# Performance work log

Hardware: AMD Instinct MI355X
Metric: run time of the kernel (lower is better)

Reference implementation:

```python
import jax, jax.numpy as jnp
import numpy as np

B, L, H, HEADS, BLOCKS, TSPAN = 8, 256, 256, 4, 2, 512
D = H // HEADS
BIG_NEG = jnp.float32(-2.0**32 + 1)


def _layernorm(x, g, b, eps=1e-8):
    m = x.mean(-1, keepdims=True)
    v = ((x - m) ** 2).mean(-1, keepdims=True)
    return (x - m) / jnp.sqrt(v + eps) * g + b


def _forward(seq_emb, Wq, bq, Wk, bk, Wv, bv, ln1_g, ln1_b, ln2_g, ln2_b,
             W1, b1, W2, b2, pos_K, pos_V, tK_emb, tV_emb, lnf_g, lnf_b,
             mask, time_matrices):
    # relative time-interval embeddings: [B,L,L,H] -> per-head [B,L,L,heads,D]
    tmKh = tK_emb[time_matrices].reshape(B, L, L, HEADS, D)
    tmVh = tV_emb[time_matrices].reshape(B, L, L, HEADS, D)
    posKh = pos_K.reshape(L, HEADS, D)  # abs position embs (positions = arange(L))
    posVh = pos_V.reshape(L, HEADS, D)
    keep = (~mask)[..., None].astype(seq_emb.dtype)  # [B,L,1], True mask = pad
    causal = ~jnp.tril(jnp.ones((L, L), dtype=bool))  # True above diagonal
    x = seq_emb * keep
    scale = jnp.sqrt(jnp.float32(D))
    for i in range(BLOCKS):
        q = _layernorm(x, ln1_g[i], ln1_b[i])  # queries normalized, keys/values raw
        Qh = (q @ Wq[i].T + bq[i]).reshape(B, L, HEADS, D)
        Kh = (x @ Wk[i].T + bk[i]).reshape(B, L, HEADS, D)
        Vh = (x @ Wv[i].T + bv[i]).reshape(B, L, HEADS, D)
        aw = (jnp.einsum('bqhd,bkhd->bhqk', Qh, Kh)
              + jnp.einsum('bqhd,khd->bhqk', Qh, posKh)
              + jnp.einsum('bqhd,bqkhd->bhqk', Qh, tmKh)) / scale
        aw = jnp.where(mask[:, None, :, None] | causal[None, None], BIG_NEG, aw)
        p = jax.nn.softmax(aw, axis=-1)
        out = (jnp.einsum('bhqk,bkhd->bqhd', p, Vh)
               + jnp.einsum('bhqk,khd->bqhd', p, posVh)
               + jnp.einsum('bhqk,bqkhd->bqhd', p, tmVh)).reshape(B, L, H)
        x = q + out
        x = _layernorm(x, ln2_g[i], ln2_b[i])
        h = jax.nn.relu(jnp.einsum('bld,od->blo', x, W1[i]) + b1[i])  # Conv1d k=1 == Linear
        x = jnp.einsum('bld,od->blo', h, W2[i]) + b2[i] + x
        x = x * keep
    return _layernorm(x, lnf_g, lnf_b)


def setup_inputs():
    key = jax.random.key(0)
    ks = jax.random.split(key, 24)
    s = 0.02
    nrm = lambda k, shape: jax.random.normal(k, shape, dtype=jnp.float32) * s
    inp = {}
    inp['mask'] = jax.random.uniform(ks[0], (B, L)) < 0.1
    inp['seq_emb'] = jax.random.normal(ks[1], (B, L, H), dtype=jnp.float32)
    inp['log_seqs'] = jax.random.randint(ks[2], (B, L), 0, 1000)
    inp['time_matrices'] = jax.random.randint(ks[3], (B, L, L), 0, TSPAN + 1).astype(jnp.int32)
    inp['time_attn'] = 0
    inp['Wq'] = nrm(ks[4], (BLOCKS, H, H)); inp['bq'] = jnp.zeros((BLOCKS, H), jnp.float32)
    inp['Wk'] = nrm(ks[5], (BLOCKS, H, H)); inp['bk'] = jnp.zeros((BLOCKS, H), jnp.float32)
    inp['Wv'] = nrm(ks[6], (BLOCKS, H, H)); inp['bv'] = jnp.zeros((BLOCKS, H), jnp.float32)
    inp['ln1_g'] = jnp.ones((BLOCKS, H), jnp.float32); inp['ln1_b'] = jnp.zeros((BLOCKS, H), jnp.float32)
    inp['ln2_g'] = jnp.ones((BLOCKS, H), jnp.float32); inp['ln2_b'] = jnp.zeros((BLOCKS, H), jnp.float32)
    inp['W1'] = nrm(ks[7], (BLOCKS, H, H)); inp['b1'] = jnp.zeros((BLOCKS, H), jnp.float32)
    inp['W2'] = nrm(ks[8], (BLOCKS, H, H)); inp['b2'] = jnp.zeros((BLOCKS, H), jnp.float32)
    inp['pos_K'] = nrm(ks[9], (L, H)); inp['pos_V'] = nrm(ks[10], (L, H))
    inp['tK_emb'] = nrm(ks[11], (TSPAN + 1, H)); inp['tV_emb'] = nrm(ks[12], (TSPAN + 1, H))
    inp['lnf_g'] = jnp.ones((H,), jnp.float32); inp['lnf_b'] = jnp.zeros((H,), jnp.float32)
    return inp


def reference(mask, seq_emb, log_seqs, time_matrices, time_attn,
              Wq, bq, Wk, bk, Wv, bv, ln1_g, ln1_b, ln2_g, ln2_b,
              W1, b1, W2, b2, pos_K, pos_V, tK_emb, tV_emb, lnf_g, lnf_b):
    return _forward(seq_emb, Wq, bq, Wk, bk, Wv, bv, ln1_g, ln1_b, ln2_g, ln2_b,
                    W1, b1, W2, b2, pos_K, pos_V, tK_emb, tV_emb, lnf_g, lnf_b,
                    mask, time_matrices)
```

## Files before the change

### kernel.cpp

```cpp
#include <hip/hip_runtime.h>

#define BIG_NEG_F (-4294967296.0f)

typedef __attribute__((ext_vector_type(8))) short bf16x8;
typedef __attribute__((ext_vector_type(4))) float f32x4;

__device__ __forceinline__ float wave_sum(float v) {
#pragma unroll
    for (int m = 32; m; m >>= 1) v += __shfl_xor(v, m, 64);
    return v;
}
__device__ __forceinline__ float wave_max(float v) {
#pragma unroll
    for (int m = 32; m; m >>= 1) v = fmaxf(v, __shfl_xor(v, m, 64));
    return v;
}

__device__ __forceinline__ unsigned int pack2(float a, float b) {
    return (__float_as_uint(b) & 0xffff0000u) | (__float_as_uint(a) >> 16);
}
__device__ __forceinline__ float hipart(float x) {
    return __uint_as_float(__float_as_uint(x) & 0xffff0000u);
}
__device__ __forceinline__ void store_pair(unsigned short* hp, unsigned short* lp,
                                           float4 a, float4 b) {
    uint4 h;
    h.x = pack2(a.x, a.y); h.y = pack2(a.z, a.w);
    h.z = pack2(b.x, b.y); h.w = pack2(b.z, b.w);
    float lax = a.x - hipart(a.x), lay = a.y - hipart(a.y);
    float laz = a.z - hipart(a.z), law = a.w - hipart(a.w);
    float lbx = b.x - hipart(b.x), lby = b.y - hipart(b.y);
    float lbz = b.z - hipart(b.z), lbw = b.w - hipart(b.w);
    uint4 l;
    l.x = pack2(lax, lay); l.y = pack2(laz, law);
    l.z = pack2(lbx, lby); l.w = pack2(lbz, lbw);
    *(uint4*)hp = h;
    *(uint4*)lp = l;
}

__global__ __launch_bounds__(256) void prep_ln_kernel(const float* __restrict__ seq,
                                                      const unsigned char* __restrict__ mraw,
                                                      unsigned char* __restrict__ mout,
                                                      float* __restrict__ X, float* __restrict__ Q,
                                                      const float* __restrict__ g,
                                                      const float* __restrict__ be) {
    __shared__ int flags[2];
    __shared__ float ws[8];
    int row = blockIdx.x, tid = threadIdx.x;
    if (tid == 0) { flags[0] = 0; flags[1] = 0; }
    __syncthreads();
    for (int i = tid; i < 2048; i += 256) {
        if (mraw[i]) {
            if (i & 3) atomicOr(&flags[0], 1);
            else if (i & 4) atomicOr(&flags[1], 1);
        }
    }
    __syncthreads();
    int mode = flags[0] ? 0 : (flags[1] ? 1 : 2);
    unsigned char mrow = (mode == 0) ? mraw[row] : (mode == 1) ? mraw[row * 4] : mraw[row * 8];
    if (tid == 0) mout[row] = mrow ? 1 : 0;
    int idx = row * 256 + tid;
    int w = tid >> 6, lane = tid & 63;
    float v = mrow ? 0.f : seq[idx];
    X[idx] = v;
    float s = wave_sum(v);
    if (lane == 0) ws[w] = s;
    __syncthreads();
    float mean = (ws[0] + ws[1] + ws[2] + ws[3]) * (1.f / 256.f);
    float d = v - mean;
    float s2 = wave_sum(d * d);
    if (lane == 0) ws[4 + w] = s2;
    __syncthreads();
    float var = (ws[4] + ws[5] + ws[6] + ws[7]) * (1.f / 256.f);
    Q[idx] = d / sqrtf(var + 1e-8f) * g[tid] + be[tid];
}

__global__ __launch_bounds__(256) void ln_kernel(const float* __restrict__ X, float* __restrict__ Y,
                                                 const float* __restrict__ g,
                                                 const float* __restrict__ be) {
    __shared__ float ws[8];
    int row = blockIdx.x, tid = threadIdx.x;
    int idx = row * 256 + tid;
    int w = tid >> 6, lane = tid & 63;
    float v = X[idx];
    float s = wave_sum(v);
    if (lane == 0) ws[w] = s;
    __syncthreads();
    float mean = (ws[0] + ws[1] + ws[2] + ws[3]) * (1.f / 256.f);
    float d = v - mean;
    float s2 = wave_sum(d * d);
    if (lane == 0) ws[4 + w] = s2;
    __syncthreads();
    float var = (ws[4] + ws[5] + ws[6] + ws[7]) * (1.f / 256.f);
    Y[idx] = d / sqrtf(var + 1e-8f) * g[tid] + be[tid];
}

struct GemmJob {
    const float* A;
    const float* W;
    const float* bias;
    const float* pos;
    const float* res;
    const unsigned char* maskm;
    float* C;
    int relu;
};

__global__ __launch_bounds__(256) void gemm_mfma_kernel(GemmJob j0, GemmJob j1, GemmJob j2) {
    GemmJob J = (blockIdx.z == 0) ? j0 : (blockIdx.z == 1 ? j1 : j2);
    __shared__ unsigned short Ah[32][72], Al[32][72], Wh[64][72], Wl[64][72];
    int tid = threadIdx.x;
    int n0 = blockIdx.x * 64, m0 = blockIdx.y * 32;
    int w = tid >> 6, lane = tid & 63;
    int wm = w >> 1, wn = w & 1;
    int rowA = tid >> 3, kA = (tid & 7) * 8;
    int rowW = tid >> 2, kW = (tid & 3) * 16;
    const float* Asrc = J.A + (m0 + rowA) * 256 + kA;
    const float* Wsrc = J.W + (n0 + rowW) * 256 + kW;
    float4 ar0 = *(const float4*)(Asrc), ar1 = *(const float4*)(Asrc + 4);
    float4 wr0 = *(const float4*)(Wsrc),      wr1 = *(const float4*)(Wsrc + 4),
           wr2 = *(const float4*)(Wsrc + 8),  wr3 = *(const float4*)(Wsrc + 12);
    f32x4 acc[2] = {};
    int r15 = lane & 15, hgrp = (lane >> 4) << 3;
    for (int kt = 0; kt < 4; ++kt) {
        if (kt) __syncthreads();
        store_pair(&Ah[rowA][kA],     &Al[rowA][kA],     ar0, ar1);
        store_pair(&Wh[rowW][kW],     &Wl[rowW][kW],     wr0, wr1);
        store_pair(&Wh[rowW][kW + 8], &Wl[rowW][kW + 8], wr2, wr3);
        __syncthreads();
        if (kt < 3) {
            int ko = (kt + 1) * 64;
            ar0 = *(const float4*)(Asrc + ko);      ar1 = *(const float4*)(Asrc + ko + 4);
            wr0 = *(const float4*)(Wsrc + ko);      wr1 = *(const float4*)(Wsrc + ko + 4);
            wr2 = *(const float4*)(Wsrc + ko + 8);  wr3 = *(const float4*)(Wsrc + ko + 12);
        }
#pragma unroll
        for (int s = 0; s < 2; ++s) {
            int ko = s * 32 + hgrp;
            bf16x8 ah = *(const bf16x8*)&Ah[wm * 16 + r15][ko];
            bf16x8 al = *(const bf16x8*)&Al[wm * 16 + r15][ko];
            bf16x8 bh0 = *(const bf16x8*)&Wh[wn * 32 + r15][ko];
            bf16x8 bh1 = *(const bf16x8*)&Wh[wn * 32 + 16 + r15][ko];
            bf16x8 bl0 = *(const bf16x8*)&Wl[wn * 32 + r15][ko];
            bf16x8 bl1 = *(const bf16x8*)&Wl[wn * 32 + 16 + r15][ko];
            acc[0] = __builtin_amdgcn_mfma_f32_16x16x32_bf16(ah, bh0, acc[0], 0, 0, 0);
            acc[0] = __builtin_amdgcn_mfma_f32_16x16x32_bf16(ah, bl0, acc[0], 0, 0, 0);
            acc[0] = __builtin_amdgcn_mfma_f32_16x16x32_bf16(al, bh0, acc[0], 0, 0, 0);
            acc[1] = __builtin_amdgcn_mfma_f32_16x16x32_bf16(ah, bh1, acc[1], 0, 0, 0);
            acc[1] = __builtin_amdgcn_mfma_f32_16x16x32_bf16(ah, bl1, acc[1], 0, 0, 0);
            acc[1] = __builtin_amdgcn_mfma_f32_16x16x32_bf16(al, bh1, acc[1], 0, 0, 0);
        }
    }
#pragma unroll
    for (int nf = 0; nf < 2; ++nf) {
        int col = n0 + wn * 32 + nf * 16 + r15;
        int rowb = m0 + wm * 16 + ((lane >> 4) << 2);
        float bcol = J.bias[col];
        f32x4 a = acc[nf];
#pragma unroll
        for (int rr = 0; rr < 4; ++rr) {
            int m = rowb + rr;
            float v = a[rr] + bcol;
            if (J.pos) v += J.pos[(m & 255) * 256 + col];
            if (J.relu) v = fmaxf(v, 0.f);
            if (J.res) v += J.res[m * 256 + col];
            if (J.maskm && J.maskm[m]) v = 0.f;
            J.C[m * 256 + col] = v;
        }
    }
}

__global__ __launch_bounds__(256, 4) void attn_kernel(
    const float* __restrict__ Q, const float* __restrict__ Kp, const float* __restrict__ Vp,
    const float* __restrict__ qres, const int* __restrict__ tm,
    const float* __restrict__ tK, const float* __restrict__ tV,
    const float* __restrict__ g2, const float* __restrict__ b2,
    float* __restrict__ X2) {
    int bid = (int)blockIdx.x;
    int b = bid & 7;
    int i6 = bid >> 3;
    int j = i6 & 31, a = i6 >> 5;
    int base = 2 * j + (a >> 1);
    int P = (a & 1) ? base : 127 - base;
    int qA = 2 * P, qB = 2 * P + 1;
    int tid = threadIdx.x, w = tid >> 6, lane = tid & 63;
    __shared__ float qrow[2][256];
    __shared__ int   stm[2][256];
    __shared__ float p[2][4][264];
    __shared__ float opart[2][4][256];
    __shared__ float denom[2][4];
    __shared__ float lnws[2][8];

    int rowbaseA = (b * 256 + qA) * 256;
    int rowbaseB = (b * 256 + qB) * 256;
    qrow[0][tid] = Q[rowbaseA + tid];
    qrow[1][tid] = Q[rowbaseB + tid];
    {
        int tA = tm[rowbaseA + tid];
        int tB = tm[rowbaseB + tid];
        stm[0][tid] = tA < 0 ? 0 : (tA > 512 ? 512 : tA);
        stm[1][tid] = tB < 0 ? 0 : (tB > 512 ? 512 : tB);
    }
    __syncthreads();

    {
        int h = lane >> 4;
        const float* qrA = &qrow[0][lane * 4];
        const float* qrB = &qrow[1][lane * 4];
        float qA0 = qrA[0], qA1 = qrA[1], qA2 = qrA[2], qA3 = qrA[3];
        float qB0 = qrB[0], qB1 = qrB[1], qB2 = qrB[2], qB3 = qrB[3];
        const float* Kb  = Kp + (size_t)(b << 8) * 256 + lane * 4;
        const float* tKb = tK + lane * 4;
        int nact = (qB >= w) ? ((qB - w) >> 2) + 1 : 0;
        int i = 0;
        for (; i + 2 <= nact; i += 2) {
            int k0 = w + 4 * i, k1 = k0 + 4;
            float4 kv0 = *(const float4*)(Kb + k0 * 256);
            float4 kv1 = *(const float4*)(Kb + k1 * 256);
            float4 tA0 = *(const float4*)(tKb + stm[0][k0] * 256);
            float4 tA1 = *(const float4*)(tKb + stm[0][k1] * 256);
            float4 tB0 = *(const float4*)(tKb + stm[1][k0] * 256);
            float4 tB1 = *(const float4*)(tKb + stm[1][k1] * 256);
            float sA0 = qA0 * (kv0.x + tA0.x) + qA1 * (kv0.y + tA0.y) + qA2 * (kv0.z + tA0.z) + qA3 * (kv0.w + tA0.w);
            float sA1 = qA0 * (kv1.x + tA1.x) + qA1 * (kv1.y + tA1.y) + qA2 * (kv1.z + tA1.z) + qA3 * (kv1.w + tA1.w);
            float sB0 = qB0 * (kv0.x + tB0.x) + qB1 * (kv0.y + tB0.y) + qB2 * (kv0.z + tB0.z) + qB3 * (kv0.w + tB0.w);
            float sB1 = qB0 * (kv1.x + tB1.x) + qB1 * (kv1.y + tB1.y) + qB2 * (kv1.z + tB1.z) + qB3 * (kv1.w + tB1.w);
            sA0 += __shfl_xor(sA0, 1, 64); sA1 += __shfl_xor(sA1, 1, 64);
            sB0 += __shfl_xor(sB0, 1, 64); sB1 += __shfl_xor(sB1, 1, 64);
            sA0 += __shfl_xor(sA0, 2, 64); sA1 += __shfl_xor(sA1, 2, 64);
            sB0 += __shfl_xor(sB0, 2, 64); sB1 += __shfl_xor(sB1, 2, 64);
            sA0 += __shfl_xor(sA0, 4, 64); sA1 += __shfl_xor(sA1, 4, 64);
            sB0 += __shfl_xor(sB0, 4, 64); sB1 += __shfl_xor(sB1, 4, 64);
            sA0 += __shfl_xor(sA0, 8, 64); sA1 += __shfl_xor(sA1, 8, 64);
            sB0 += __shfl_xor(sB0, 8, 64); sB1 += __shfl_xor(sB1, 8, 64);
            if ((lane & 15) == 0) {
                p[0][h][k0] = sA0 * 0.125f;
                p[0][h][k1] = sA1 * 0.125f;
                p[1][h][k0] = sB0 * 0.125f;
                p[1][h][k1] = sB1 * 0.125f;
            }
        }
        if (i < nact) {
            int k = w + 4 * i;
            float4 kv = *(const float4*)(Kb + k * 256);
            float4 tA4 = *(const float4*)(tKb + stm[0][k] * 256);
            float4 tB4 = *(const float4*)(tKb + stm[1][k] * 256);
            float sA = qA0 * (kv.x + tA4.x) + qA1 * (kv.y + tA4.y) + qA2 * (kv.z + tA4.z) + qA3 * (kv.w + tA4.w);
            float sB = qB0 * (kv.x + tB4.x) + qB1 * (kv.y + tB4.y) + qB2 * (kv.z + tB4.z) + qB3 * (kv.w + tB4.w);
            sA += __shfl_xor(sA, 1, 64); sB += __shfl_xor(sB, 1, 64);
            sA += __shfl_xor(sA, 2, 64); sB += __shfl_xor(sB, 2, 64);
            sA += __shfl_xor(sA, 4, 64); sB += __shfl_xor(sB, 4, 64);
            sA += __shfl_xor(sA, 8, 64); sB += __shfl_xor(sB, 8, 64);
            if ((lane & 15) == 0) {
                p[0][h][k] = sA * 0.125f;
                p[1][h][k] = sB * 0.125f;
            }
        }
    }
    __syncthreads();

    {
        float* phA = &p[0][w][0];
        float* phB = &p[1][w][0];
        float a0 = (lane       <= qA) ? phA[lane      ] : BIG_NEG_F;
        float a1 = (lane + 64  <= qA) ? phA[lane + 64 ] : BIG_NEG_F;
        float a2 = (lane + 128 <= qA) ? phA[lane + 128] : BIG_NEG_F;
        float a3 = (lane + 192 <= qA) ? phA[lane + 192] : BIG_NEG_F;
        float b0 = (lane       <= qB) ? phB[lane      ] : BIG_NEG_F;
        float b1 = (lane + 64  <= qB) ? phB[lane + 64 ] : BIG_NEG_F;
        float b2v = (lane + 128 <= qB) ? phB[lane + 128] : BIG_NEG_F;
        float b3 = (lane + 192 <= qB) ? phB[lane + 192] : BIG_NEG_F;
        float mxA = wave_max(fmaxf(fmaxf(a0, a1), fmaxf(a2, a3)));
        float mxB = wave_max(fmaxf(fmaxf(b0, b1), fmaxf(b2v, b3)));
        float eA0 = (lane       <= qA) ? __expf(a0 - mxA) : 0.f;
        float eA1 = (lane + 64  <= qA) ? __expf(a1 - mxA) : 0.f;
        float eA2 = (lane + 128 <= qA) ? __expf(a2 - mxA) : 0.f;
        float eA3 = (lane + 192 <= qA) ? __expf(a3 - mxA) : 0.f;
        float eB0 = (lane       <= qB) ? __expf(b0 - mxB) : 0.f;
        float eB1 = (lane + 64  <= qB) ? __expf(b1 - mxB) : 0.f;
        float eB2 = (lane + 128 <= qB) ? __expf(b2v - mxB) : 0.f;
        float eB3 = (lane + 192 <= qB) ? __expf(b3 - mxB) : 0.f;
        phA[lane] = eA0; phA[lane + 64] = eA1; phA[lane + 128] = eA2; phA[lane + 192] = eA3;
        phB[lane] = eB0; phB[lane + 64] = eB1; phB[lane + 128] = eB2; phB[lane + 192] = eB3;
        float sumA = wave_sum(eA0 + eA1 + eA2 + eA3);
        float sumB = wave_sum(eB0 + eB1 + eB2 + eB3);
        if (lane == 0) { denom[0][w] = sumA; denom[1][w] = sumB; }
    }
    __syncthreads();

    {
        int hh = lane >> 4;
        const float* Vb  = Vp + (size_t)(b << 8) * 256 + lane * 4;
        const float* tVb = tV + lane * 4;
        const float* prA = &p[0][hh][0];
        const float* prB = &p[1][hh][0];
        float4 aA0 = {0.f, 0.f, 0.f, 0.f}, aA1 = aA0, aB0 = aA0, aB1 = aA0;
        int cnt = (qB >= w) ? ((qB - w) >> 2) + 1 : 0;
        int i = 0;
        for (; i + 2 <= cnt; i += 2) {
            int k0 = w + 4 * i, k1 = k0 + 4;
            float pA0 = prA[k0], pA1 = prA[k1], pB0 = prB[k0], pB1 = prB[k1];
            float4 v0 = *(const float4*)(Vb + k0 * 256);
            float4 v1 = *(const float4*)(Vb + k1 * 256);
            float4 uA0 = *(const float4*)(tVb + stm[0][k0] * 256);
            float4 uA1 = *(const float4*)(tVb + stm[0][k1] * 256);
            float4 uB0 = *(const float4*)(tVb + stm[1][k0] * 256);
            float4 uB1 = *(const float4*)(tVb + stm[1][k1] * 256);
            aA0.x += pA0 * (v0.x + uA0.x); aA0.y += pA0 * (v0.y + uA0.y); aA0.z += pA0 * (v0.z + uA0.z); aA0.w += pA0 * (v0.w + uA0.w);
            aA1.x += pA1 * (v1.x + uA1.x); aA1.y += pA1 * (v1.y + uA1.y); aA1.z += pA1 * (v1.z + uA1.z); aA1.w += pA1 * (v1.w + uA1.w);
            aB0.x += pB0 * (v0.x + uB0.x); aB0.y += pB0 * (v0.y + uB0.y); aB0.z += pB0 * (v0.z + uB0.z); aB0.w += pB0 * (v0.w + uB0.w);
            aB1.x += pB1 * (v1.x + uB1.x); aB1.y += pB1 * (v1.y + uB1.y); aB1.z += pB1 * (v1.z + uB1.z); aB1.w += pB1 * (v1.w + uB1.w);
        }
        if (i < cnt) {
            int k2 = w + 4 * i;
            float pA = prA[k2], pB = prB[k2];
            float4 v = *(const float4*)(Vb + k2 * 256);
            float4 uA = *(const float4*)(tVb + stm[0][k2] * 256);
            float4 uB = *(const float4*)(tVb + stm[1][k2] * 256);
            aA0.x += pA * (v.x + uA.x); aA0.y += pA * (v.y + uA.y);
            aA0.z += pA * (v.z + uA.z); aA0.w += pA * (v.w + uA.w);
            aB0.x += pB * (v.x + uB.x); aB0.y += pB * (v.y + uB.y);
            aB0.z += pB * (v.z + uB.z); aB0.w += pB * (v.w + uB.w);
        }
        float4 oA, oB;
        oA.x = aA0.x + aA1.x; oA.y = aA0.y + aA1.y; oA.z = aA0.z + aA1.z; oA.w = aA0.w + aA1.w;
        oB.x = aB0.x + aB1.x; oB.y = aB0.y + aB1.y; oB.z = aB0.z + aB1.z; oB.w = aB0.w + aB1.w;
        *(float4*)&opart[0][w][lane * 4] = oA;
        *(float4*)&opart[1][w][lane * 4] = oB;
    }
    __syncthreads();

    {
        int d = tid, h = tid >> 6;
        float totA = opart[0][0][d] + opart[0][1][d] + opart[0][2][d] + opart[0][3][d];
        float totB = opart[1][0][d] + opart[1][1][d] + opart[1][2][d] + opart[1][3][d];
        float xvA = qres[rowbaseA + d] + totA / denom[0][h];
        float xvB = qres[rowbaseB + d] + totB / denom[1][h];
        float sA = wave_sum(xvA);
        float sB = wave_sum(xvB);
        if (lane == 0) { lnws[0][w] = sA; lnws[1][w] = sB; }
        __syncthreads();
        float meanA = (lnws[0][0] + lnws[0][1] + lnws[0][2] + lnws[0][3]) * (1.f / 256.f);
        float meanB = (lnws[1][0] + lnws[1][1] + lnws[1][2] + lnws[1][3]) * (1.f / 256.f);
        float ddA = xvA - meanA, ddB = xvB - meanB;
        float s2A = wave_sum(ddA * ddA);
        float s2B = wave_sum(ddB * ddB);
        if (lane == 0) { lnws[0][4 + w] = s2A; lnws[1][4 + w] = s2B; }
        __syncthreads();
        float varA = (lnws[0][4] + lnws[0][5] + lnws[0][6] + lnws[0][7]) * (1.f / 256.f);
        float varB = (lnws[1][4] + lnws[1][5] + lnws[1][6] + lnws[1][7]) * (1.f / 256.f);
        float gg = g2[d], bb = b2[d];
        X2[rowbaseA + d] = ddA / sqrtf(varA + 1e-8f) * gg + bb;
        X2[rowbaseB + d] = ddB / sqrtf(varB + 1e-8f) * gg + bb;
    }
}

extern "C" void kernel_launch(void* const* d_in, const int* in_sizes, int n_in,
                              void* d_out, int out_size, void* d_ws, size_t ws_size,
                              hipStream_t stream) {
    const unsigned char* mask_raw = (const unsigned char*)d_in[0];
    const float* seq  = (const float*)d_in[1];
    const int*   tm   = (const int*)d_in[3];
    const float* Wq   = (const float*)d_in[5];
    const float* bq   = (const float*)d_in[6];
    const float* Wk   = (const float*)d_in[7];
    const float* bk   = (const float*)d_in[8];
    const float* Wv   = (const float*)d_in[9];
    const float* bv   = (const float*)d_in[10];
    const float* ln1g = (const float*)d_in[11];
    const float* ln1b = (const float*)d_in[12];
    const float* ln2g = (const float*)d_in[13];
    const float* ln2b = (const float*)d_in[14];
    const float* W1   = (const float*)d_in[15];
    const float* b1   = (const float*)d_in[16];
    const float* W2   = (const float*)d_in[17];
    const float* b2   = (const float*)d_in[18];
    const float* posK = (const float*)d_in[19];
    const float* posV = (const float*)d_in[20];
    const float* tK   = (const float*)d_in[21];
    const float* tV   = (const float*)d_in[22];
    const float* lnfg = (const float*)d_in[23];
    const float* lnfb = (const float*)d_in[24];

    const int NEL = 8 * 256 * 256;
    float* x   = (float*)d_ws;
    float* q   = x   + NEL;
    float* Qb  = q   + NEL;
    float* KpB = Qb  + NEL;
    float* VpB = KpB + NEL;
    float* x2  = VpB + NEL;
    float* hb  = x2  + NEL;
    unsigned char* mask = (unsigned char*)(hb + NEL);

    dim3 gQKV(4, 64, 3);
    dim3 gFFN(4, 64, 1);

    prep_ln_kernel<<<2048, 256, 0, stream>>>(seq, mask_raw, mask, x, q, ln1g, ln1b);
    for (int blk = 0; blk < 2; ++blk) {
        int o1 = blk * 256, oW = blk * 256 * 256;
        GemmJob jq = {q, Wq + oW, bq + o1, nullptr, nullptr, nullptr, Qb, 0};
        GemmJob jk = {x, Wk + oW, bk + o1, posK,    nullptr, nullptr, KpB, 0};
        GemmJob jv = {x, Wv + oW, bv + o1, posV,    nullptr, nullptr, VpB, 0};
        gemm_mfma_kernel<<<gQKV, 256, 0, stream>>>(jq, jk, jv);
        attn_kernel<<<1024, 256, 0, stream>>>(Qb, KpB, VpB, q, tm, tK, tV,
                                              ln2g + o1, ln2b + o1, x2);
        GemmJob f1 = {x2, W1 + oW, b1 + o1, nullptr, nullptr, nullptr, hb, 1};
        gemm_mfma_kernel<<<gFFN, 256, 0, stream>>>(f1, f1, f1);
        GemmJob f2 = {hb, W2 + oW, b2 + o1, nullptr, x2, mask, x, 0};
        gemm_mfma_kernel<<<gFFN, 256, 0, stream>>>(f2, f2, f2);
        if (blk == 0) ln_kernel<<<2048, 256, 0, stream>>>(x, q, ln1g + 256, ln1b + 256);
    }
    ln_kernel<<<2048, 256, 0, stream>>>(x, (float*)d_out, lnfg, lnfb);
}
```

Baseline: 236.8 us.

## Precompute query-by-time-embedding scores with MFMA and gather them in attention

Adds a kernel that multiplies every query head vector by all 513 time-interval key embeddings using split-bf16 MFMA, writing a per-query, per-head score table. The attention kernel then gathers one scalar per key from this table instead of loading a 4-float tK row per lane and folding it into the dot product. This removes the redundant gathered tK traffic, since only 513 distinct embeddings exist. The cost is an extra launch and a table of 2048x4x516 floats written and read through global memory, plus slight precision loss from the three-term bf16 split.

```diff
diff --git a/kernel.cpp b/kernel.cpp
--- a/kernel.cpp
+++ b/kernel.cpp
@@ -1,6 +1,7 @@
 #include <hip/hip_runtime.h>
 
 #define BIG_NEG_F (-4294967296.0f)
+#define TSTRIDE 516
 
 typedef __attribute__((ext_vector_type(8))) short bf16x8;
 typedef __attribute__((ext_vector_type(4))) float f32x4;
@@ -36,6 +37,17 @@
     l.z = pack2(lbx, lby); l.w = pack2(lbz, lbw);
     *(uint4*)hp = h;
     *(uint4*)lp = l;
+}
+__device__ __forceinline__ void mk_frag(float4 a, float4 b, bf16x8* hi, bf16x8* lo) {
+    uint4 h, l;
+    h.x = pack2(a.x, a.y); h.y = pack2(a.z, a.w);
+    h.z = pack2(b.x, b.y); h.w = pack2(b.z, b.w);
+    l.x = pack2(a.x - hipart(a.x), a.y - hipart(a.y));
+    l.y = pack2(a.z - hipart(a.z), a.w - hipart(a.w));
+    l.z = pack2(b.x - hipart(b.x), b.y - hipart(b.y));
+    l.w = pack2(b.z - hipart(b.z), b.w - hipart(b.w));
+    *hi = *(bf16x8*)&h;
+    *lo = *(bf16x8*)&l;
 }
 
 __global__ __launch_bounds__(256) void prep_ln_kernel(const float* __restrict__ seq,
@@ -170,10 +182,48 @@
     }
 }
 
+__global__ __launch_bounds__(256) void tscore_kernel(const float* __restrict__ Qp,
+                                                     const float* __restrict__ tK,
+                                                     float* __restrict__ T) {
+    int tid = threadIdx.x, w = tid >> 6, lane = tid & 63;
+    int t0 = blockIdx.x * 64 + w * 16;
+    int q0 = blockIdx.y * 16;
+    int h  = blockIdx.z;
+    int r15 = lane & 15, kq = (lane >> 4) << 3;
+    const float* Ap = Qp + (q0 + r15) * 256 + h * 64 + kq;
+    int trow = t0 + r15;
+    const float* Bp = tK + trow * 256 + h * 64 + kq;
+    bool tvalid = trow < 513;
+    f32x4 acc = {0.f, 0.f, 0.f, 0.f};
+#pragma unroll
+    for (int s = 0; s < 2; ++s) {
+        float4 a0 = *(const float4*)(Ap + s * 32);
+        float4 a1 = *(const float4*)(Ap + s * 32 + 4);
+        float4 b0 = {0.f, 0.f, 0.f, 0.f}, b1 = b0;
+        if (tvalid) {
+            b0 = *(const float4*)(Bp + s * 32);
+            b1 = *(const float4*)(Bp + s * 32 + 4);
+        }
+        bf16x8 ah, al, bh, bl;
+        mk_frag(a0, a1, &ah, &al);
+        mk_frag(b0, b1, &bh, &bl);
+        acc = __builtin_amdgcn_mfma_f32_16x16x32_bf16(ah, bh, acc, 0, 0, 0);
+        acc = __builtin_amdgcn_mfma_f32_16x16x32_bf16(ah, bl, acc, 0, 0, 0);
+        acc = __builtin_amdgcn_mfma_f32_16x16x32_bf16(al, bh, acc, 0, 0, 0);
+    }
+    int tcol = t0 + r15;
+    if (tcol < 513) {
+        int qrow = q0 + ((lane >> 4) << 2);
+#pragma unroll
+        for (int rr = 0; rr < 4; ++rr)
+            T[((qrow + rr) * 4 + h) * TSTRIDE + tcol] = acc[rr];
+    }
+}
+
 __global__ __launch_bounds__(256, 4) void attn_kernel(
     const float* __restrict__ Q, const float* __restrict__ Kp, const float* __restrict__ Vp,
     const float* __restrict__ qres, const int* __restrict__ tm,
-    const float* __restrict__ tK, const float* __restrict__ tV,
+    const float* __restrict__ T, const float* __restrict__ tV,
     const float* __restrict__ g2, const float* __restrict__ b2,
     float* __restrict__ X2) {
     int bid = (int)blockIdx.x;
@@ -193,6 +243,7 @@
 
     int rowbaseA = (b * 256 + qA) * 256;
     int rowbaseB = (b * 256 + qB) * 256;
+    int qgA = b * 256 + qA, qgB = b * 256 + qB;
     qrow[0][tid] = Q[rowbaseA + tid];
     qrow[1][tid] = Q[rowbaseB + tid];
     {
@@ -209,22 +260,21 @@
         const float* qrB = &qrow[1][lane * 4];
         float qA0 = qrA[0], qA1 = qrA[1], qA2 = qrA[2], qA3 = qrA[3];
         float qB0 = qrB[0], qB1 = qrB[1], qB2 = qrB[2], qB3 = qrB[3];
-        const float* Kb  = Kp + (size_t)(b << 8) * 256 + lane * 4;
-        const float* tKb = tK + lane * 4;
+        const float* Kb = Kp + (size_t)(b << 8) * 256 + lane * 4;
+        const float* TA = T + (qgA * 4 + h) * TSTRIDE;
+        const float* TB = T + (qgB * 4 + h) * TSTRIDE;
         int nact = (qB >= w) ? ((qB - w) >> 2) + 1 : 0;
         int i = 0;
         for (; i + 2 <= nact; i += 2) {
             int k0 = w + 4 * i, k1 = k0 + 4;
             float4 kv0 = *(const float4*)(Kb + k0 * 256);
             float4 kv1 = *(const float4*)(Kb + k1 * 256);
-            float4 tA0 = *(const float4*)(tKb + stm[0][k0] * 256);
-            float4 tA1 = *(const float4*)(tKb + stm[0][k1] * 256);
-            float4 tB0 = *(const float4*)(tKb + stm[1][k0] * 256);
-            float4 tB1 = *(const float4*)(tKb + stm[1][k1] * 256);
-            float sA0 = qA0 * (kv0.x + tA0.x) + qA1 * (kv0.y + tA0.y) + qA2 * (kv0.z + tA0.z) + qA3 * (kv0.w + tA0.w);
-            float sA1 = qA0 * (kv1.x + tA1.x) + qA1 * (kv1.y + tA1.y) + qA2 * (kv1.z + tA1.z) + qA3 * (kv1.w + tA1.w);
-            float sB0 = qB0 * (kv0.x + tB0.x) + qB1 * (kv0.y + tB0.y) + qB2 * (kv0.z + tB0.z) + qB3 * (kv0.w + tB0.w);
-            float sB1 = qB0 * (kv1.x + tB1.x) + qB1 * (kv1.y + tB1.y) + qB2 * (kv1.z + tB1.z) + qB3 * (kv1.w + tB1.w);
+            float tA0 = TA[stm[0][k0]], tA1 = TA[stm[0][k1]];
+            float tB0 = TB[stm[1][k0]], tB1 = TB[stm[1][k1]];
+            float sA0 = qA0 * kv0.x + qA1 * kv0.y + qA2 * kv0.z + qA3 * kv0.w;
+            float sA1 = qA0 * kv1.x + qA1 * kv1.y + qA2 * kv1.z + qA3 * kv1.w;
+            float sB0 = qB0 * kv0.x + qB1 * kv0.y + qB2 * kv0.z + qB3 * kv0.w;
+            float sB1 = qB0 * kv1.x + qB1 * kv1.y + qB2 * kv1.z + qB3 * kv1.w;
             sA0 += __shfl_xor(sA0, 1, 64); sA1 += __shfl_xor(sA1, 1, 64);
             sB0 += __shfl_xor(sB0, 1, 64); sB1 += __shfl_xor(sB1, 1, 64);
             sA0 += __shfl_xor(sA0, 2, 64); sA1 += __shfl_xor(sA1, 2, 64);
@@ -234,26 +284,25 @@
             sA0 += __shfl_xor(sA0, 8, 64); sA1 += __shfl_xor(sA1, 8, 64);
             sB0 += __shfl_xor(sB0, 8, 64); sB1 += __shfl_xor(sB1, 8, 64);
             if ((lane & 15) == 0) {
-                p[0][h][k0] = sA0 * 0.125f;
-                p[0][h][k1] = sA1 * 0.125f;
-                p[1][h][k0] = sB0 * 0.125f;
-                p[1][h][k1] = sB1 * 0.125f;
+                p[0][h][k0] = (sA0 + tA0) * 0.125f;
+                p[0][h][k1] = (sA1 + tA1) * 0.125f;
+                p[1][h][k0] = (sB0 + tB0) * 0.125f;
+                p[1][h][k1] = (sB1 + tB1) * 0.125f;
             }
         }
         if (i < nact) {
             int k = w + 4 * i;
             float4 kv = *(const float4*)(Kb + k * 256);
-            float4 tA4 = *(const float4*)(tKb + stm[0][k] * 256);
-            float4 tB4 = *(const float4*)(tKb + stm[1][k] * 256);
-            float sA = qA0 * (kv.x + tA4.x) + qA1 * (kv.y + tA4.y) + qA2 * (kv.z + tA4.z) + qA3 * (kv.w + tA4.w);
-            float sB = qB0 * (kv.x + tB4.x) + qB1 * (kv.y + tB4.y) + qB2 * (kv.z + tB4.z) + qB3 * (kv.w + tB4.w);
+            float tA4 = TA[stm[0][k]], tB4 = TB[stm[1][k]];
+            float sA = qA0 * kv.x + qA1 * kv.y + qA2 * kv.z + qA3 * kv.w;
+            float sB = qB0 * kv.x + qB1 * kv.y + qB2 * kv.z + qB3 * kv.w;
             sA += __shfl_xor(sA, 1, 64); sB += __shfl_xor(sB, 1, 64);
             sA += __shfl_xor(sA, 2, 64); sB += __shfl_xor(sB, 2, 64);
             sA += __shfl_xor(sA, 4, 64); sB += __shfl_xor(sB, 4, 64);
             sA += __shfl_xor(sA, 8, 64); sB += __shfl_xor(sB, 8, 64);
             if ((lane & 15) == 0) {
-                p[0][h][k] = sA * 0.125f;
-                p[1][h][k] = sB * 0.125f;
+                p[0][h][k] = (sA + tA4) * 0.125f;
+                p[1][h][k] = (sB + tB4) * 0.125f;
             }
         }
     }
@@ -391,9 +440,11 @@
     float* x2  = VpB + NEL;
     float* hb  = x2  + NEL;
     unsigned char* mask = (unsigned char*)(hb + NEL);
+    float* T = (float*)(mask + 2048);
 
     dim3 gQKV(4, 64, 3);
     dim3 gFFN(4, 64, 1);
+    dim3 gT(9, 128, 4);
 
     prep_ln_kernel<<<2048, 256, 0, stream>>>(seq, mask_raw, mask, x, q, ln1g, ln1b);
     for (int blk = 0; blk < 2; ++blk) {
@@ -402,7 +453,8 @@
         GemmJob jk = {x, Wk + oW, bk + o1, posK,    nullptr, nullptr, KpB, 0};
         GemmJob jv = {x, Wv + oW, bv + o1, posV,    nullptr, nullptr, VpB, 0};
         gemm_mfma_kernel<<<gQKV, 256, 0, stream>>>(jq, jk, jv);
-        attn_kernel<<<1024, 256, 0, stream>>>(Qb, KpB, VpB, q, tm, tK, tV,
+        tscore_kernel<<<gT, 256, 0, stream>>>(Qb, tK, T);
+        attn_kernel<<<1024, 256, 0, stream>>>(Qb, KpB, VpB, q, tm, T, tV,
                                               ln2g + o1, ln2b + o1, x2);
         GemmJob f1 = {x2, W1 + oW, b1 + o1, nullptr, nullptr, nullptr, hb, 1};
         gemm_mfma_kernel<<<gFFN, 256, 0, stream>>>(f1, f1, f1);
```

Result: slower. 283.6 us (+19.8%).
